# Kernel optimization log

Measured on AMD Instinct MI355X. Metric: run time of the kernel, lower is better.

## Reference

```python
import jax, jax.numpy as jnp
import numpy as np

KERNEL = 128
STRIDE = 64


def setup_inputs() -> dict:
    key = jax.random.key(0)
    k1, k2, k3 = jax.random.split(key, 3)
    in_features = 8192
    fold_num = (in_features - KERNEL) // STRIDE + 1  # 127
    local_features = 128
    batch = 2048
    x = jax.random.normal(k1, (batch, in_features), dtype=jnp.float32)
    # stacked per-window Linear weights/biases (PyTorch Linear: y = x @ W.T + b)
    bound = 1.0 / np.sqrt(KERNEL)
    W = jax.random.uniform(k2, (fold_num, local_features, KERNEL), dtype=jnp.float32,
                           minval=-bound, maxval=bound)
    b = jax.random.uniform(k3, (fold_num, local_features), dtype=jnp.float32,
                           minval=-bound, maxval=bound)
    return {"x": x, "W": W, "b": b}


def reference(x, W, b):
    fold_num = W.shape[0]
    # window gather indices: [fold_num, kernel]
    idx = STRIDE * jnp.arange(fold_num)[:, None] + jnp.arange(KERNEL)[None, :]
    windows = x[:, idx]                      # [batch, fold_num, kernel]
    # per-window linear: out[b,f,l] = sum_k windows[b,f,k] * W[f,l,k] + b[f,l]
    out = jnp.einsum('bfk,flk->bfl', windows, W) + b[None, :, :]
    # concat along feature dim as in torch.cat(..., 1)
    return out.reshape(out.shape[0], -1)     # [batch, fold_num*local_features]
```

## Files before the change

### kernel.cpp

```cpp
#include <hip/hip_runtime.h>
#include <hip/hip_bf16.h>

typedef float f32x4 __attribute__((ext_vector_type(4)));
typedef __bf16 bf16x8 __attribute__((ext_vector_type(8)));

#define INF   8192
#define FOLDS 127
#define LOCAL 128
#define OUTF  (FOLDS * LOCAL)
#define BM    64
#define BN    64

__device__ __forceinline__ void cvt_store8(char* lds, int byte, f32x4 v0, f32x4 v1) {
    bf16x8 w;
    w[0] = (__bf16)v0[0]; w[1] = (__bf16)v0[1]; w[2] = (__bf16)v0[2]; w[3] = (__bf16)v0[3];
    w[4] = (__bf16)v1[0]; w[5] = (__bf16)v1[1]; w[6] = (__bf16)v1[2]; w[7] = (__bf16)v1[3];
    *(bf16x8*)(lds + byte) = w;
}

__global__ __launch_bounds__(256, 5)
void local_linear_kernel(const float* __restrict__ x,
                         const float* __restrict__ W,
                         const float* __restrict__ bias,
                         float* __restrict__ out)
{
    __shared__ __align__(16) __bf16 As[BM * 128];
    __shared__ __align__(16) __bf16 Bs[BN * 128];

    const int mt = blockIdx.x;
    const int fn = blockIdx.y;
    const int f  = fn >> 1;
    const int bn0 = (fn & 1) * BN;
    const int t  = threadIdx.x;

    const int m0   = mt * BM;
    const int lane = t & 63;
    const int wid  = t >> 6;
    const int wm   = wid >> 1;
    const int wn   = wid & 1;
    const int r16  = lane & 15;
    const int kq   = lane >> 4;

    const float* __restrict__ Wf = W + (size_t)f * (LOCAL * 128) + (size_t)bn0 * 128;
    #pragma unroll
    for (int it = 0; it < 4; ++it) {
        const int e   = it * 2048 + t * 8;
        const int row = e >> 7;
        const int col = e & 127;
        const float* g = Wf + row * 128 + col;
        f32x4 v0 = *(const f32x4*)g;
        f32x4 v1 = *(const f32x4*)(g + 4);
        cvt_store8((char*)Bs, (row * 256 + col * 2) ^ ((row & 7) << 4), v0, v1);
    }

    const float* __restrict__ xg = x + (size_t)m0 * INF + (size_t)f * 64;
    #pragma unroll
    for (int it = 0; it < 4; ++it) {
        const int e   = it * 2048 + t * 8;
        const int row = e >> 7;
        const int col = e & 127;
        const float* g = xg + (size_t)row * INF + col;
        f32x4 v0 = *(const f32x4*)g;
        f32x4 v1 = *(const f32x4*)(g + 4);
        cvt_store8((char*)As, (row * 256 + col * 2) ^ ((row & 7) << 4), v0, v1);
    }
    __syncthreads();

    float bv[2];
    #pragma unroll
    for (int j = 0; j < 2; ++j)
        bv[j] = bias[f * LOCAL + bn0 + wn * 32 + j * 16 + r16];

    f32x4 acc[2][2];
    #pragma unroll
    for (int i = 0; i < 2; ++i)
        #pragma unroll
        for (int j = 0; j < 2; ++j)
            acc[i][j] = (f32x4){bv[j], bv[j], bv[j], bv[j]};

    #pragma unroll
    for (int ks = 0; ks < 4; ++ks) {
        const int kof = ks * 32 + kq * 8;
        bf16x8 a[2], b[2];
        #pragma unroll
        for (int i = 0; i < 2; ++i) {
            const int row  = wm * 32 + i * 16 + r16;
            const int byte = (row * 256 + kof * 2) ^ ((row & 7) << 4);
            a[i] = *(const bf16x8*)((const char*)As + byte);
        }
        #pragma unroll
        for (int j = 0; j < 2; ++j) {
            const int row  = wn * 32 + j * 16 + r16;
            const int byte = (row * 256 + kof * 2) ^ ((row & 7) << 4);
            b[j] = *(const bf16x8*)((const char*)Bs + byte);
        }
        #pragma unroll
        for (int i = 0; i < 2; ++i)
            #pragma unroll
            for (int j = 0; j < 2; ++j)
                acc[i][j] = __builtin_amdgcn_mfma_f32_16x16x32_bf16(a[i], b[j], acc[i][j], 0, 0, 0);
    }

    #pragma unroll
    for (int i = 0; i < 2; ++i) {
        const int mrow = m0 + wm * 32 + i * 16 + kq * 4;
        #pragma unroll
        for (int j = 0; j < 2; ++j) {
            const int ncol = f * LOCAL + bn0 + wn * 32 + j * 16 + r16;
            float* o = out + (size_t)mrow * OUTF + ncol;
            #pragma unroll
            for (int r = 0; r < 4; ++r)
                o[(size_t)r * OUTF] = acc[i][j][r];
        }
    }
}

extern "C" void kernel_launch(void* const* d_in, const int* in_sizes, int n_in,
                              void* d_out, int out_size, void* d_ws, size_t ws_size,
                              hipStream_t stream) {
    const float* x    = (const float*)d_in[0];
    const float* W    = (const float*)d_in[1];
    const float* bias = (const float*)d_in[2];
    float* out        = (float*)d_out;

    dim3 grid(2048 / BM, FOLDS * 2);
    dim3 block(256);
    local_linear_kernel<<<grid, block, 0, stream>>>(x, W, bias, out);
}
```

Before: 46.81 us.

## Persist blocks over batch tiles with double-buffered async global-to-LDS x loads

Each block now loops over eight batch tiles for one fold/half, loading and converting W into LDS only once. The x tiles arrive fp32 in LDS through global_load_lds direct copies into a double buffer, so the next tile loads while the current one computes. Conversion to bf16 moves into the fragment read path. This cuts repeated W traffic and per-block launch overhead, but doubles x LDS footprint, lowers occupancy to 2 blocks per CU, and relies on hand-tuned vmcnt waits whose counts must match the outstanding loads.

```diff
diff --git a/kernel.cpp b/kernel.cpp
--- a/kernel.cpp
+++ b/kernel.cpp
@@ -10,6 +10,8 @@
 #define OUTF  (FOLDS * LOCAL)
 #define BM    64
 #define BN    64
+#define NT    8
+#define NBG   (2048 / (BM * NT))
 
 __device__ __forceinline__ void cvt_store8(char* lds, int byte, f32x4 v0, f32x4 v1) {
     bf16x8 w;
@@ -18,22 +20,21 @@
     *(bf16x8*)(lds + byte) = w;
 }
 
-__global__ __launch_bounds__(256, 5)
+__global__ __launch_bounds__(256, 2)
 void local_linear_kernel(const float* __restrict__ x,
                          const float* __restrict__ W,
                          const float* __restrict__ bias,
                          float* __restrict__ out)
 {
-    __shared__ __align__(16) __bf16 As[BM * 128];
+    __shared__ __align__(16) float  Ax[2][BM * 128];
     __shared__ __align__(16) __bf16 Bs[BN * 128];
 
-    const int mt = blockIdx.x;
-    const int fn = blockIdx.y;
-    const int f  = fn >> 1;
+    const int bg  = blockIdx.x;
+    const int fn  = blockIdx.y;
+    const int f   = fn >> 1;
     const int bn0 = (fn & 1) * BN;
-    const int t  = threadIdx.x;
+    const int t   = threadIdx.x;
 
-    const int m0   = mt * BM;
     const int lane = t & 63;
     const int wid  = t >> 6;
     const int wm   = wid >> 1;
@@ -41,77 +42,110 @@
     const int r16  = lane & 15;
     const int kq   = lane >> 4;
 
+    const float* __restrict__ xf = x + (size_t)f * 64;
+
+    auto stage_x = [&](int buf, int tile) {
+        const size_t row0 = (size_t)(bg * NT + tile) * BM;
+        char* dstbase = (char*)Ax[buf];
+        #pragma unroll
+        for (int c = 0; c < 8; ++c) {
+            const int base = c * 4096 + wid * 1024;
+            const int b    = base + lane * 16;
+            const int row  = b >> 9;
+            const int srci = (b & 511) ^ ((row & 7) << 4);
+            const char* src = (const char*)(xf + (row0 + row) * INF) + srci;
+            __builtin_amdgcn_global_load_lds(
+                (const __attribute__((address_space(1))) void*)src,
+                (__attribute__((address_space(3))) void*)(dstbase + base),
+                16, 0, 0);
+        }
+    };
+
+    stage_x(0, 0);
+
     const float* __restrict__ Wf = W + (size_t)f * (LOCAL * 128) + (size_t)bn0 * 128;
     #pragma unroll
     for (int it = 0; it < 4; ++it) {
-        const int e   = it * 2048 + t * 8;
-        const int row = e >> 7;
-        const int col = e & 127;
+        const int e = it * 2048 + t * 8;
+        const int row = e >> 7, col = e & 127;
         const float* g = Wf + row * 128 + col;
         f32x4 v0 = *(const f32x4*)g;
         f32x4 v1 = *(const f32x4*)(g + 4);
         cvt_store8((char*)Bs, (row * 256 + col * 2) ^ ((row & 7) << 4), v0, v1);
     }
 
-    const float* __restrict__ xg = x + (size_t)m0 * INF + (size_t)f * 64;
-    #pragma unroll
-    for (int it = 0; it < 4; ++it) {
-        const int e   = it * 2048 + t * 8;
-        const int row = e >> 7;
-        const int col = e & 127;
-        const float* g = xg + (size_t)row * INF + col;
-        f32x4 v0 = *(const f32x4*)g;
-        f32x4 v1 = *(const f32x4*)(g + 4);
-        cvt_store8((char*)As, (row * 256 + col * 2) ^ ((row & 7) << 4), v0, v1);
-    }
-    __syncthreads();
-
     float bv[2];
     #pragma unroll
     for (int j = 0; j < 2; ++j)
         bv[j] = bias[f * LOCAL + bn0 + wn * 32 + j * 16 + r16];
 
-    f32x4 acc[2][2];
-    #pragma unroll
-    for (int i = 0; i < 2; ++i)
-        #pragma unroll
-        for (int j = 0; j < 2; ++j)
-            acc[i][j] = (f32x4){bv[j], bv[j], bv[j], bv[j]};
+    __syncthreads();
 
     #pragma unroll
-    for (int ks = 0; ks < 4; ++ks) {
-        const int kof = ks * 32 + kq * 8;
-        bf16x8 a[2], b[2];
-        #pragma unroll
-        for (int i = 0; i < 2; ++i) {
-            const int row  = wm * 32 + i * 16 + r16;
-            const int byte = (row * 256 + kof * 2) ^ ((row & 7) << 4);
-            a[i] = *(const bf16x8*)((const char*)As + byte);
+    for (int tt = 0; tt < NT; ++tt) {
+        if (tt + 1 < NT) {
+            stage_x((tt + 1) & 1, tt + 1);
+            if (tt == 0) asm volatile("s_waitcnt vmcnt(8)"  ::: "memory");
+            else         asm volatile("s_waitcnt vmcnt(24)" ::: "memory");
+        } else {
+            asm volatile("s_waitcnt vmcnt(16)" ::: "memory");
         }
-        #pragma unroll
-        for (int j = 0; j < 2; ++j) {
-            const int row  = wn * 32 + j * 16 + r16;
-            const int byte = (row * 256 + kof * 2) ^ ((row & 7) << 4);
-            b[j] = *(const bf16x8*)((const char*)Bs + byte);
-        }
+        __builtin_amdgcn_s_barrier();
+        __builtin_amdgcn_sched_barrier(0);
+
+        const int cb = tt & 1;
+        f32x4 acc[2][2];
         #pragma unroll
         for (int i = 0; i < 2; ++i)
             #pragma unroll
             for (int j = 0; j < 2; ++j)
-                acc[i][j] = __builtin_amdgcn_mfma_f32_16x16x32_bf16(a[i], b[j], acc[i][j], 0, 0, 0);
-    }
+                acc[i][j] = (f32x4){bv[j], bv[j], bv[j], bv[j]};
 
-    #pragma unroll
-    for (int i = 0; i < 2; ++i) {
-        const int mrow = m0 + wm * 32 + i * 16 + kq * 4;
         #pragma unroll
-        for (int j = 0; j < 2; ++j) {
-            const int ncol = f * LOCAL + bn0 + wn * 32 + j * 16 + r16;
-            float* o = out + (size_t)mrow * OUTF + ncol;
+        for (int ks = 0; ks < 4; ++ks) {
+            const int kof2 = ks * 128 + kq * 32;
+            bf16x8 a[2], b[2];
             #pragma unroll
-            for (int r = 0; r < 4; ++r)
-                o[(size_t)r * OUTF] = acc[i][j][r];
+            for (int i = 0; i < 2; ++i) {
+                const int row = wm * 32 + i * 16 + r16;
+                const int sw  = (row & 7) << 4;
+                const char* p = (const char*)Ax[cb] + row * 512;
+                f32x4 u = *(const f32x4*)(p + ((kof2 +  0) ^ sw));
+                f32x4 v = *(const f32x4*)(p + ((kof2 + 16) ^ sw));
+                bf16x8 w;
+                w[0] = (__bf16)u[0]; w[1] = (__bf16)u[1]; w[2] = (__bf16)u[2]; w[3] = (__bf16)u[3];
+                w[4] = (__bf16)v[0]; w[5] = (__bf16)v[1]; w[6] = (__bf16)v[2]; w[7] = (__bf16)v[3];
+                a[i] = w;
+            }
+            #pragma unroll
+            for (int j = 0; j < 2; ++j) {
+                const int row  = wn * 32 + j * 16 + r16;
+                const int byte = (row * 256 + (ks * 32 + kq * 8) * 2) ^ ((row & 7) << 4);
+                b[j] = *(const bf16x8*)((const char*)Bs + byte);
+            }
+            #pragma unroll
+            for (int i = 0; i < 2; ++i)
+                #pragma unroll
+                for (int j = 0; j < 2; ++j)
+                    acc[i][j] = __builtin_amdgcn_mfma_f32_16x16x32_bf16(a[i], b[j], acc[i][j], 0, 0, 0);
         }
+
+        const int m0 = (bg * NT + tt) * BM;
+        #pragma unroll
+        for (int i = 0; i < 2; ++i) {
+            const int mrow = m0 + wm * 32 + i * 16 + kq * 4;
+            #pragma unroll
+            for (int j = 0; j < 2; ++j) {
+                const int ncol = f * LOCAL + bn0 + wn * 32 + j * 16 + r16;
+                float* o = out + (size_t)mrow * OUTF + ncol;
+                #pragma unroll
+                for (int r = 0; r < 4; ++r)
+                    o[(size_t)r * OUTF] = acc[i][j][r];
+            }
+        }
+
+        __builtin_amdgcn_sched_barrier(0);
+        __builtin_amdgcn_s_barrier();
     }
 }
 
@@ -123,7 +157,7 @@
     const float* bias = (const float*)d_in[2];
     float* out        = (float*)d_out;
 
-    dim3 grid(2048 / BM, FOLDS * 2);
+    dim3 grid(NBG, FOLDS * 2);
     dim3 block(256);
     local_linear_kernel<<<grid, block, 0, stream>>>(x, W, bias, out);
 }
```

Result: slower. 53.16 us (+13.6%).
